# Kernel tuning notes

Measured on AMD Instinct MI355X. Metric: run time of the kernel, lower is better.

Reference implementation:

```python
import jax, jax.numpy as jnp
import numpy as np
from jax import lax

EMB, H1, H2 = 100, 128, 64  # embedding_dim, hidden_dim, hidden_dim//2
B, T = 1024, 512


def _uniform(key, shape, scale):
    return jax.random.uniform(key, shape, jnp.float32, -scale, scale)


def setup_inputs() -> dict:
    key = jax.random.key(0)
    ks = jax.random.split(key, 16)
    s1 = 1.0 / np.sqrt(H1)
    s2 = 1.0 / np.sqrt(H2)
    return {
        "X": jax.random.normal(ks[0], (B, T, EMB), jnp.float32),
        # PyTorch LSTM weights, gate order (i, f, g, o)
        "W1_ih": _uniform(ks[1], (4 * H1, EMB), s1),
        "W1_hh": _uniform(ks[2], (4 * H1, H1), s1),
        "b1_ih": _uniform(ks[3], (4 * H1,), s1),
        "b1_hh": _uniform(ks[4], (4 * H1,), s1),
        "W2_ih": _uniform(ks[5], (4 * H2, H1), s2),
        "W2_hh": _uniform(ks[6], (4 * H2, H2), s2),
        "b2_ih": _uniform(ks[7], (4 * H2,), s2),
        "b2_hh": _uniform(ks[8], (4 * H2,), s2),
        "fc1_w": _uniform(ks[9], (32, H2), 1.0 / np.sqrt(H2)),
        "fc1_b": _uniform(ks[10], (32,), 1.0 / np.sqrt(H2)),
        "fc2_w": _uniform(ks[11], (1, 32), 1.0 / np.sqrt(32)),
        "fc2_b": _uniform(ks[12], (1,), 1.0 / np.sqrt(32)),
    }


def _lstm(x, W_ih, W_hh, b_ih, b_hh):
    # x: [B, T, D]; returns (all hidden states [B, T, H], final h [B, H])
    Bb = x.shape[0]
    H = W_hh.shape[1]
    # Batch the input projection across all timesteps (one big GEMM).
    xw = jnp.einsum('btd,gd->tbg', x, W_ih) + (b_ih + b_hh)  # [T, B, 4H]

    def step(carry, xt):
        h, c = carry
        gates = xt + h @ W_hh.T  # [B, 4H]
        i, f, g, o = jnp.split(gates, 4, axis=-1)
        c = jax.nn.sigmoid(f) * c + jax.nn.sigmoid(i) * jnp.tanh(g)
        h = jax.nn.sigmoid(o) * jnp.tanh(c)
        return (h, c), h

    h0 = jnp.zeros((Bb, H), x.dtype)
    (h_n, _), hs = lax.scan(step, (h0, h0), xw)
    return jnp.swapaxes(hs, 0, 1), h_n


def reference(X, W1_ih, W1_hh, b1_ih, b1_hh,
              W2_ih, W2_hh, b2_ih, b2_hh,
              fc1_w, fc1_b, fc2_w, fc2_b):
    hs1, _ = _lstm(X, W1_ih, W1_hh, b1_ih, b1_hh)        # [B, T, 128]
    # dropout is identity at inference
    _, h_n = _lstm(hs1, W2_ih, W2_hh, b2_ih, b2_hh)      # [B, 64]
    x = jax.nn.relu(h_n @ fc1_w.T + fc1_b)               # [B, 32]
    x = x @ fc2_w.T + fc2_b                              # [B, 1]
    return jax.nn.sigmoid(x)[:, 0]                       # [B]
```

## Files before the change

### kernel.cpp

```cpp
#include <hip/hip_runtime.h>
#include <hip/hip_fp16.h>

typedef _Float16 half8 __attribute__((ext_vector_type(8)));
typedef _Float16 half4 __attribute__((ext_vector_type(4)));
typedef float floatx4 __attribute__((ext_vector_type(4)));

#define TT 512
#define EE 100
#define NBATCH 16
#define NBLK 64
#define WS_NEED ((size_t)NBLK * TT * 2048 * sizeof(_Float16))

typedef const __attribute__((address_space(1))) void gvoid_t;
typedef __attribute__((address_space(3))) void lvoid_t;

#define MFMA16 __builtin_amdgcn_mfma_f32_16x16x32_f16

__device__ __forceinline__ float sigm(float x) {
    return __builtin_amdgcn_rcpf(1.0f + __expf(-x));
}
__device__ __forceinline__ float tanh_(float x) {
    return __builtin_amdgcn_rcpf(1.0f + __expf(-2.0f * x)) * 2.0f - 1.0f;
}
__device__ __forceinline__ half4 cvt4(float4 v) {
    half4 h; h[0] = (_Float16)v.x; h[1] = (_Float16)v.y; h[2] = (_Float16)v.z; h[3] = (_Float16)v.w;
    return h;
}

extern "C" __global__ void __launch_bounds__(256)
xfrag_prep(const float* __restrict__ X, _Float16* __restrict__ xw)
{
    const int bt  = blockIdx.x;
    const int blk = bt >> 9;
    const int t   = bt & (TT - 1);
    const int tid = threadIdx.x;
    const int c   = tid >> 4, m = tid & 15;
    const int k0  = 8 * c;
    half8 v;
#pragma unroll
    for (int j = 0; j < 8; ++j) v[j] = (_Float16)0.0f;
    const float* p = X + ((size_t)(blk * 16 + m) * TT + t) * EE + k0;
    if (k0 + 8 <= EE) {
        float4 lo = *(const float4*)p;
        float4 hi = *(const float4*)(p + 4);
        v[0] = (_Float16)lo.x; v[1] = (_Float16)lo.y; v[2] = (_Float16)lo.z; v[3] = (_Float16)lo.w;
        v[4] = (_Float16)hi.x; v[5] = (_Float16)hi.y; v[6] = (_Float16)hi.z; v[7] = (_Float16)hi.w;
    } else if (k0 < EE) {
        float4 lo = *(const float4*)p;
        v[0] = (_Float16)lo.x; v[1] = (_Float16)lo.y; v[2] = (_Float16)lo.z; v[3] = (_Float16)lo.w;
        v[4] = (_Float16)1.0f;
    }
    *(half8*)&xw[(size_t)bt * 2048 + c * 128 + m * 8] = v;
}

template<int USE_WS>
__global__ void __launch_bounds__(512, 1)
lstm_mfma4(const float* __restrict__ X, const _Float16* __restrict__ xw,
           const float* __restrict__ W1ih, const float* __restrict__ W1hh,
           const float* __restrict__ b1i,  const float* __restrict__ b1h,
           const float* __restrict__ W2ih, const float* __restrict__ W2hh,
           const float* __restrict__ b2i,  const float* __restrict__ b2h,
           const float* __restrict__ fc1w, const float* __restrict__ fc1b,
           const float* __restrict__ fc2w, const float* __restrict__ fc2b,
           float* __restrict__ out)
{
    const int tid  = threadIdx.x;
    const int w    = tid >> 6;
    const int lane = tid & 63;
    const int q    = lane >> 4;
    const int m    = lane & 15;
    const int b0   = blockIdx.x * NBATCH;

    __shared__ __align__(16) _Float16 h1b[2][4][4][16][8];
    __shared__ __align__(16) _Float16 h2b[2][2][4][16][8];
    __shared__ __align__(16) _Float16 xb [2][4][4][16][8];
    __shared__ float fca[NBATCH][32];

    _Float16* const h1f = &h1b[0][0][0][0][0];
    _Float16* const h2f = &h2b[0][0][0][0][0];
    _Float16* const xbf = &xb [0][0][0][0][0];

    for (int i = tid; i < 2 * 2048; i += 512) h1f[i] = (_Float16)0.0f;
    for (int i = tid; i < 2 * 1024; i += 512) h2f[i] = (_Float16)0.0f;
    if (!USE_WS) {
        for (int i = tid; i < 2 * 2048; i += 512) {
            const int k = i & 2047;
            xbf[i] = (k >= 1536 && k < 1664 && (k & 7) == 4) ? (_Float16)1.0f
                                                             : (_Float16)0.0f;
        }
    }

    half8 w1ihf[4][4], w1hhf[4][4], w2ihf[2][4], w2hhf[2][2];
    floatx4 bias2v[2];
#pragma unroll
    for (int g = 0; g < 4; ++g) {
        const int r = g * 128 + 16 * w + m;
        const float bias = b1i[r] + b1h[r];
#pragma unroll
        for (int s = 0; s < 4; ++s) {
            half8 f;
#pragma unroll
            for (int j = 0; j < 8; ++j) {
                const int k = 32 * s + 8 * q + j;
                float v = 0.0f;
                if (k < EE) v = W1ih[r * EE + k];
                else if (k == EE) v = bias;
                f[j] = (_Float16)v;
            }
            w1ihf[g][s] = f;
        }
#pragma unroll
        for (int s = 0; s < 4; ++s) {
            half8 f;
#pragma unroll
            for (int j = 0; j < 8; ++j) f[j] = (_Float16)W1hh[r * 128 + 32 * s + 8 * q + j];
            w1hhf[g][s] = f;
        }
    }
#pragma unroll
    for (int tau = 0; tau < 2; ++tau) {
        const int rr = (m & 3) * 64 + 8 * w + 4 * tau + (m >> 2);
#pragma unroll
        for (int s = 0; s < 4; ++s) {
            half8 f;
#pragma unroll
            for (int j = 0; j < 8; ++j) f[j] = (_Float16)W2ih[rr * 128 + 32 * s + 8 * q + j];
            w2ihf[tau][s] = f;
        }
#pragma unroll
        for (int s = 0; s < 2; ++s) {
            half8 f;
#pragma unroll
            for (int j = 0; j < 8; ++j) f[j] = (_Float16)W2hh[rr * 64 + 32 * s + 8 * q + j];
            w2hhf[tau][s] = f;
        }
        const int uu = 8 * w + 4 * tau + q;
#pragma unroll
        for (int reg = 0; reg < 4; ++reg)
            bias2v[tau][reg] = b2i[reg * 64 + uu] + b2h[reg * 64 + uu];
    }

    const _Float16* xwb = xw + (size_t)blockIdx.x * TT * 2048;
    const int foff = q * 128 + m * 8;

    int gaddr = 0, laddr = 0;
    bool xval = false;
    float4 xr = {0.f, 0.f, 0.f, 0.f};
    if (!USE_WS) {
        xval = tid < 400;
        const int f = xval ? tid : 0;
        const int n = f / 25, pp = f - 25 * n, e0 = 4 * pp;
        gaddr = (b0 + n) * (TT * EE) + e0;
        const int s = e0 >> 5, qr = (e0 >> 3) & 3, j0 = e0 & 7;
        laddr = ((s * 4 + qr) * 16 + n) * 8 + j0;
    }

    __syncthreads();

    if (USE_WS) {
        if (w < 4) {
            __builtin_amdgcn_global_load_lds((gvoid_t*)(xwb + 0 * 2048 + w * 512 + lane * 8),
                                             (lvoid_t*)(xbf + 0 * 2048 + w * 512), 16, 0, 0);
            __builtin_amdgcn_global_load_lds((gvoid_t*)(xwb + 1 * 2048 + w * 512 + lane * 8),
                                             (lvoid_t*)(xbf + 1 * 2048 + w * 512), 16, 0, 0);
        }
    } else if (xval) {
        *(half4*)&xbf[0 * 2048 + laddr] = cvt4(*(const float4*)&X[gaddr + 0 * EE]);
        *(half4*)&xbf[1 * 2048 + laddr] = cvt4(*(const float4*)&X[gaddr + 1 * EE]);
        xr = *(const float4*)&X[gaddr + 2 * EE];
    }
    __syncthreads();

    floatx4 a1x[4];
#pragma unroll
    for (int g = 0; g < 4; ++g) a1x[g] = (floatx4){0.f, 0.f, 0.f, 0.f};
    {
        const _Float16* xc = xbf + 0 * 2048 + foff;
#pragma unroll
        for (int s = 0; s < 4; ++s) {
            half8 bx = *(const half8*)(xc + s * 512);
#pragma unroll
            for (int g = 0; g < 4; ++g) a1x[g] = MFMA16(w1ihf[g][s], bx, a1x[g], 0, 0, 0);
        }
    }

    floatx4 c1 = {0.f, 0.f, 0.f, 0.f};
    float c2[2] = {0.f, 0.f};
    const int vv = 2 * w + (q >> 1);
    const int jj = 4 * (q & 1);

#pragma unroll 1
    for (int t = 0; t < TT; ++t) {
        const int cur = t & 1, nxt = cur ^ 1;

        {
            const _Float16* hp = h1f + nxt * 2048 + foff;
#pragma unroll
            for (int s = 0; s < 4; ++s) {
                half8 bh = *(const half8*)(hp + s * 512);
#pragma unroll
                for (int g = 0; g < 4; ++g)
                    a1x[g] = MFMA16(w1hhf[g][s], bh, a1x[g], 0, 0, 0);
            }
        }
        {
            half4 hv;
#pragma unroll
            for (int r = 0; r < 4; ++r) {
                const float iv = sigm(a1x[0][r]);
                const float fv = sigm(a1x[1][r]);
                const float gv = tanh_(a1x[2][r]);
                const float ov = sigm(a1x[3][r]);
                const float c  = fv * c1[r] + iv * gv;
                c1[r] = c;
                hv[r] = (_Float16)(ov * tanh_(c));
            }
            *(half4*)&h1b[cur][vv >> 2][vv & 3][m][jj] = hv;
        }
        __syncthreads();

        if (USE_WS) {
            if (w < 4) {
                const int tn = (t + 2 < TT) ? (t + 2) : (TT - 1);
                __builtin_amdgcn_global_load_lds((gvoid_t*)(xwb + (size_t)tn * 2048 + w * 512 + lane * 8),
                                                 (lvoid_t*)(xbf + cur * 2048 + w * 512), 16, 0, 0);
            }
        } else if (xval) {
            *(half4*)&xbf[cur * 2048 + laddr] = cvt4(xr);
            const int tn = (t + 3 < TT) ? (t + 3) : (TT - 1);
            xr = *(const float4*)&X[gaddr + tn * EE];
        }

        floatx4 a2[2] = { bias2v[0], bias2v[1] };
        {
            const _Float16* hc = h1f + cur * 2048 + foff;
#pragma unroll
            for (int s = 0; s < 4; ++s) {
                half8 bh = *(const half8*)(hc + s * 512);
                a2[0] = MFMA16(w2ihf[0][s], bh, a2[0], 0, 0, 0);
                a2[1] = MFMA16(w2ihf[1][s], bh, a2[1], 0, 0, 0);
            }
            const _Float16* h2p = h2f + nxt * 1024 + foff;
#pragma unroll
            for (int s = 0; s < 2; ++s) {
                half8 b2v = *(const half8*)(h2p + s * 512);
                a2[0] = MFMA16(w2hhf[0][s], b2v, a2[0], 0, 0, 0);
                a2[1] = MFMA16(w2hhf[1][s], b2v, a2[1], 0, 0, 0);
            }
        }

        {
            const _Float16* xc = xbf + nxt * 2048 + foff;
#pragma unroll
            for (int g = 0; g < 4; ++g) a1x[g] = (floatx4){0.f, 0.f, 0.f, 0.f};
#pragma unroll
            for (int s = 0; s < 4; ++s) {
                half8 bx = *(const half8*)(xc + s * 512);
#pragma unroll
                for (int g = 0; g < 4; ++g)
                    a1x[g] = MFMA16(w1ihf[g][s], bx, a1x[g], 0, 0, 0);
            }
        }

#pragma unroll
        for (int tau = 0; tau < 2; ++tau) {
            const float iv = sigm(a2[tau][0]);
            const float fv = sigm(a2[tau][1]);
            const float gv = tanh_(a2[tau][2]);
            const float ov = sigm(a2[tau][3]);
            const float c  = fv * c2[tau] + iv * gv;
            c2[tau] = c;
            const int u = 8 * w + 4 * tau + q;
            h2f[cur * 1024 + (u >> 5) * 512 + ((u >> 3) & 3) * 128 + m * 8 + (u & 7)]
                = (_Float16)(ov * tanh_(c));
        }
    }
    __syncthreads();

    {
        const int nb = tid >> 5, o = tid & 31;
        float s = fc1b[o];
#pragma unroll
        for (int k = 0; k < 64; ++k)
            s += fc1w[o * 64 + k] * (float)h2b[1][k >> 5][(k >> 3) & 3][nb][k & 7];
        fca[nb][o] = fmaxf(s, 0.0f);
    }
    __syncthreads();
    if (tid < NBATCH) {
        float s = fc2b[0];
#pragma unroll
        for (int k = 0; k < 32; ++k) s += fc2w[k] * fca[tid][k];
        out[b0 + tid] = sigm(s);
    }
}

extern "C" void kernel_launch(void* const* d_in, const int* in_sizes, int n_in,
                              void* d_out, int out_size, void* d_ws, size_t ws_size,
                              hipStream_t stream) {
    const float* X    = (const float*)d_in[0];
    const float* W1ih = (const float*)d_in[1];
    const float* W1hh = (const float*)d_in[2];
    const float* b1i  = (const float*)d_in[3];
    const float* b1h  = (const float*)d_in[4];
    const float* W2ih = (const float*)d_in[5];
    const float* W2hh = (const float*)d_in[6];
    const float* b2i  = (const float*)d_in[7];
    const float* b2h  = (const float*)d_in[8];
    const float* fc1w = (const float*)d_in[9];
    const float* fc1b = (const float*)d_in[10];
    const float* fc2w = (const float*)d_in[11];
    const float* fc2b = (const float*)d_in[12];
    _Float16* xw = (_Float16*)d_ws;

    if (ws_size >= WS_NEED) {
        hipLaunchKernelGGL(xfrag_prep, dim3(NBLK * TT), dim3(256), 0, stream, X, xw);
        hipLaunchKernelGGL(lstm_mfma4<1>, dim3(NBLK), dim3(512), 0, stream,
                           X, xw, W1ih, W1hh, b1i, b1h, W2ih, W2hh, b2i, b2h,
                           fc1w, fc1b, fc2w, fc2b, (float*)d_out);
    } else {
        hipLaunchKernelGGL(lstm_mfma4<0>, dim3(NBLK), dim3(512), 0, stream,
                           X, xw, W1ih, W1hh, b1i, b1h, W2ih, W2hh, b2i, b2h,
                           fc1w, fc1b, fc2w, fc2b, (float*)d_out);
    }
}
```

Measured before the change: 1.128 ms.

## Interleave two independent batch groups per block to hide recurrence latency

Each block now runs two 16-sample batch groups (A and B) whose layer-1 and layer-2 steps are staggered by half a step, so independent MFMA and activation work from one group fills the dependency stalls of the other. This halves the grid to 32 blocks and keeps two barriers per step. The input-prep kernel is also rewritten to stage a 16-timestep tile in LDS so global reads of X are coalesced. The costs are more register pressure, only 32 of the GPU's compute units in use, and a longer serial instruction stream per block.

```diff
diff --git a/kernel.cpp b/kernel.cpp
--- a/kernel.cpp
+++ b/kernel.cpp
@@ -7,9 +7,8 @@
 
 #define TT 512
 #define EE 100
-#define NBATCH 16
-#define NBLK 64
-#define WS_NEED ((size_t)NBLK * TT * 2048 * sizeof(_Float16))
+#define NBLK 32
+#define WS_NEED ((size_t)64 * TT * 2048 * sizeof(_Float16))
 
 typedef const __attribute__((address_space(1))) void gvoid_t;
 typedef __attribute__((address_space(3))) void lvoid_t;
@@ -30,63 +29,148 @@
 extern "C" __global__ void __launch_bounds__(256)
 xfrag_prep(const float* __restrict__ X, _Float16* __restrict__ xw)
 {
-    const int bt  = blockIdx.x;
-    const int blk = bt >> 9;
-    const int t   = bt & (TT - 1);
+    const int g   = blockIdx.x >> 5;
+    const int t0  = (blockIdx.x & 31) << 4;
     const int tid = threadIdx.x;
-    const int c   = tid >> 4, m = tid & 15;
-    const int k0  = 8 * c;
-    half8 v;
-#pragma unroll
-    for (int j = 0; j < 8; ++j) v[j] = (_Float16)0.0f;
-    const float* p = X + ((size_t)(blk * 16 + m) * TT + t) * EE + k0;
-    if (k0 + 8 <= EE) {
-        float4 lo = *(const float4*)p;
-        float4 hi = *(const float4*)(p + 4);
-        v[0] = (_Float16)lo.x; v[1] = (_Float16)lo.y; v[2] = (_Float16)lo.z; v[3] = (_Float16)lo.w;
-        v[4] = (_Float16)hi.x; v[5] = (_Float16)hi.y; v[6] = (_Float16)hi.z; v[7] = (_Float16)hi.w;
-    } else if (k0 < EE) {
-        float4 lo = *(const float4*)p;
-        v[0] = (_Float16)lo.x; v[1] = (_Float16)lo.y; v[2] = (_Float16)lo.z; v[3] = (_Float16)lo.w;
-        v[4] = (_Float16)1.0f;
-    }
-    *(half8*)&xw[(size_t)bt * 2048 + c * 128 + m * 8] = v;
+
+    __shared__ __align__(16) _Float16 tile[16][16][120];
+
+    for (int mm = 0; mm < 16; ++mm) {
+        const float4* src = (const float4*)(X + ((size_t)(g * 16 + mm) * TT + t0) * EE);
+#pragma unroll
+        for (int r = 0; r < 2; ++r) {
+            const int idx = tid + r * 256;
+            if (idx < 400) {
+                float4 v = src[idx];
+                const int tt = idx / 25, kk = idx - 25 * tt;
+                *(half4*)&tile[tt][mm][4 * kk] = cvt4(v);
+            }
+        }
+    }
+    __syncthreads();
+
+    const int c = tid >> 4, mm = tid & 15;
+    for (int tt = 0; tt < 16; ++tt) {
+        half8 v;
+        if (c < 12) {
+            v = *(const half8*)&tile[tt][mm][8 * c];
+        } else if (c == 12) {
+            half4 lo = *(const half4*)&tile[tt][mm][96];
+            v[0] = lo[0]; v[1] = lo[1]; v[2] = lo[2]; v[3] = lo[3];
+            v[4] = (_Float16)1.0f;
+            v[5] = (_Float16)0.0f; v[6] = (_Float16)0.0f; v[7] = (_Float16)0.0f;
+        } else {
+#pragma unroll
+            for (int j = 0; j < 8; ++j) v[j] = (_Float16)0.0f;
+        }
+        *(half8*)&xw[((size_t)(g * TT) + t0 + tt) * 2048 + c * 128 + mm * 8] = v;
+    }
+}
+
+__device__ __forceinline__ void L1STEP(const _Float16* __restrict__ xslot,
+                                       const _Float16* __restrict__ hprev,
+                                       _Float16* __restrict__ hout,
+                                       floatx4& c1,
+                                       const half8 (&wih)[4][4], const half8 (&whh)[4][4],
+                                       int foff)
+{
+    floatx4 a[4];
+#pragma unroll
+    for (int gg = 0; gg < 4; ++gg) a[gg] = (floatx4){0.f, 0.f, 0.f, 0.f};
+#pragma unroll
+    for (int s = 0; s < 4; ++s) {
+        half8 bx = *(const half8*)(xslot + s * 512 + foff);
+#pragma unroll
+        for (int gg = 0; gg < 4; ++gg) a[gg] = MFMA16(wih[gg][s], bx, a[gg], 0, 0, 0);
+    }
+#pragma unroll
+    for (int s = 0; s < 4; ++s) {
+        half8 bh = *(const half8*)(hprev + s * 512 + foff);
+#pragma unroll
+        for (int gg = 0; gg < 4; ++gg) a[gg] = MFMA16(whh[gg][s], bh, a[gg], 0, 0, 0);
+    }
+    half4 hv;
+#pragma unroll
+    for (int r = 0; r < 4; ++r) {
+        const float iv = sigm(a[0][r]);
+        const float fv = sigm(a[1][r]);
+        const float gv = tanh_(a[2][r]);
+        const float ov = sigm(a[3][r]);
+        const float c  = fv * c1[r] + iv * gv;
+        c1[r] = c;
+        hv[r] = (_Float16)(ov * tanh_(c));
+    }
+    *(half4*)hout = hv;
+}
+
+__device__ __forceinline__ void L2STEP(const _Float16* __restrict__ h1cur,
+                                       const _Float16* __restrict__ h2prev,
+                                       _Float16* __restrict__ h2out_base,
+                                       const int (&uoff)[2],
+                                       float (&c2)[2],
+                                       const half8 (&wih)[2][4], const half8 (&whh)[2][2],
+                                       const floatx4 (&bias)[2],
+                                       int foff)
+{
+    floatx4 a2[2] = { bias[0], bias[1] };
+#pragma unroll
+    for (int s = 0; s < 4; ++s) {
+        half8 bh = *(const half8*)(h1cur + s * 512 + foff);
+        a2[0] = MFMA16(wih[0][s], bh, a2[0], 0, 0, 0);
+        a2[1] = MFMA16(wih[1][s], bh, a2[1], 0, 0, 0);
+    }
+#pragma unroll
+    for (int s = 0; s < 2; ++s) {
+        half8 bv = *(const half8*)(h2prev + s * 512 + foff);
+        a2[0] = MFMA16(whh[0][s], bv, a2[0], 0, 0, 0);
+        a2[1] = MFMA16(whh[1][s], bv, a2[1], 0, 0, 0);
+    }
+#pragma unroll
+    for (int tau = 0; tau < 2; ++tau) {
+        const float iv = sigm(a2[tau][0]);
+        const float fv = sigm(a2[tau][1]);
+        const float gv = tanh_(a2[tau][2]);
+        const float ov = sigm(a2[tau][3]);
+        const float c  = fv * c2[tau] + iv * gv;
+        c2[tau] = c;
+        h2out_base[uoff[tau]] = (_Float16)(ov * tanh_(c));
+    }
 }
 
 template<int USE_WS>
 __global__ void __launch_bounds__(512, 1)
-lstm_mfma4(const float* __restrict__ X, const _Float16* __restrict__ xw,
-           const float* __restrict__ W1ih, const float* __restrict__ W1hh,
-           const float* __restrict__ b1i,  const float* __restrict__ b1h,
-           const float* __restrict__ W2ih, const float* __restrict__ W2hh,
-           const float* __restrict__ b2i,  const float* __restrict__ b2h,
-           const float* __restrict__ fc1w, const float* __restrict__ fc1b,
-           const float* __restrict__ fc2w, const float* __restrict__ fc2b,
-           float* __restrict__ out)
+lstm_dual(const float* __restrict__ X, const _Float16* __restrict__ xw,
+          const float* __restrict__ W1ih, const float* __restrict__ W1hh,
+          const float* __restrict__ b1i,  const float* __restrict__ b1h,
+          const float* __restrict__ W2ih, const float* __restrict__ W2hh,
+          const float* __restrict__ b2i,  const float* __restrict__ b2h,
+          const float* __restrict__ fc1w, const float* __restrict__ fc1b,
+          const float* __restrict__ fc2w, const float* __restrict__ fc2b,
+          float* __restrict__ out)
 {
     const int tid  = threadIdx.x;
     const int w    = tid >> 6;
     const int lane = tid & 63;
     const int q    = lane >> 4;
     const int m    = lane & 15;
-    const int b0   = blockIdx.x * NBATCH;
-
-    __shared__ __align__(16) _Float16 h1b[2][4][4][16][8];
-    __shared__ __align__(16) _Float16 h2b[2][2][4][16][8];
-    __shared__ __align__(16) _Float16 xb [2][4][4][16][8];
-    __shared__ float fca[NBATCH][32];
-
-    _Float16* const h1f = &h1b[0][0][0][0][0];
-    _Float16* const h2f = &h2b[0][0][0][0][0];
-    _Float16* const xbf = &xb [0][0][0][0][0];
-
-    for (int i = tid; i < 2 * 2048; i += 512) h1f[i] = (_Float16)0.0f;
-    for (int i = tid; i < 2 * 1024; i += 512) h2f[i] = (_Float16)0.0f;
+    const int b0   = blockIdx.x * 32;
+
+    __shared__ __align__(16) _Float16 h1A[2 * 2048];
+    __shared__ __align__(16) _Float16 h1B[2 * 2048];
+    __shared__ __align__(16) _Float16 h2A[2 * 1024];
+    __shared__ __align__(16) _Float16 h2B[2 * 1024];
+    __shared__ __align__(16) _Float16 xbA[2 * 2048];
+    __shared__ __align__(16) _Float16 xbB[2 * 2048];
+    __shared__ float fca[32][32];
+
+    for (int i = tid; i < 2 * 2048; i += 512) { h1A[i] = (_Float16)0.0f; h1B[i] = (_Float16)0.0f; }
+    for (int i = tid; i < 2 * 1024; i += 512) { h2A[i] = (_Float16)0.0f; h2B[i] = (_Float16)0.0f; }
     if (!USE_WS) {
         for (int i = tid; i < 2 * 2048; i += 512) {
             const int k = i & 2047;
-            xbf[i] = (k >= 1536 && k < 1664 && (k & 7) == 4) ? (_Float16)1.0f
-                                                             : (_Float16)0.0f;
+            const _Float16 v = (k >= 1536 && k < 1664 && (k & 7) == 4) ? (_Float16)1.0f
+                                                                       : (_Float16)0.0f;
+            xbA[i] = v; xbB[i] = v;
         }
     }
 
@@ -140,17 +224,29 @@
             bias2v[tau][reg] = b2i[reg * 64 + uu] + b2h[reg * 64 + uu];
     }
 
-    const _Float16* xwb = xw + (size_t)blockIdx.x * TT * 2048;
-    const int foff = q * 128 + m * 8;
-
-    int gaddr = 0, laddr = 0;
+    const int foff  = q * 128 + m * 8;
+    const int vv    = 2 * w + (q >> 1);
+    const int jj    = 4 * (q & 1);
+    const int woff1 = (vv >> 2) * 512 + (vv & 3) * 128 + m * 8 + jj;
+    int uoff[2];
+#pragma unroll
+    for (int tau = 0; tau < 2; ++tau) {
+        const int u = 8 * w + 4 * tau + q;
+        uoff[tau] = (u >> 5) * 512 + ((u >> 3) & 3) * 128 + m * 8 + (u & 7);
+    }
+
+    const _Float16* xwbA = xw + (size_t)(2 * blockIdx.x)     * TT * 2048;
+    const _Float16* xwbB = xw + (size_t)(2 * blockIdx.x + 1) * TT * 2048;
+
+    int gaddrA = 0, gaddrB = 0, laddr = 0;
     bool xval = false;
-    float4 xr = {0.f, 0.f, 0.f, 0.f};
+    float4 xrA = {0.f, 0.f, 0.f, 0.f}, xrB = {0.f, 0.f, 0.f, 0.f};
     if (!USE_WS) {
         xval = tid < 400;
         const int f = xval ? tid : 0;
         const int n = f / 25, pp = f - 25 * n, e0 = 4 * pp;
-        gaddr = (b0 + n) * (TT * EE) + e0;
+        gaddrA = (b0 + n)      * (TT * EE) + e0;
+        gaddrB = (b0 + 16 + n) * (TT * EE) + e0;
         const int s = e0 >> 5, qr = (e0 >> 3) & 3, j0 = e0 & 7;
         laddr = ((s * 4 + qr) * 16 + n) * 8 + j0;
     }
@@ -159,134 +255,91 @@
 
     if (USE_WS) {
         if (w < 4) {
-            __builtin_amdgcn_global_load_lds((gvoid_t*)(xwb + 0 * 2048 + w * 512 + lane * 8),
-                                             (lvoid_t*)(xbf + 0 * 2048 + w * 512), 16, 0, 0);
-            __builtin_amdgcn_global_load_lds((gvoid_t*)(xwb + 1 * 2048 + w * 512 + lane * 8),
-                                             (lvoid_t*)(xbf + 1 * 2048 + w * 512), 16, 0, 0);
+            __builtin_amdgcn_global_load_lds((gvoid_t*)(xwbA + 0 * 2048 + w * 512 + lane * 8),
+                                             (lvoid_t*)(xbA + 0 * 2048 + w * 512), 16, 0, 0);
+            __builtin_amdgcn_global_load_lds((gvoid_t*)(xwbA + 1 * 2048 + w * 512 + lane * 8),
+                                             (lvoid_t*)(xbA + 1 * 2048 + w * 512), 16, 0, 0);
+        } else {
+            const int wb = w - 4;
+            __builtin_amdgcn_global_load_lds((gvoid_t*)(xwbB + 0 * 2048 + wb * 512 + lane * 8),
+                                             (lvoid_t*)(xbB + 0 * 2048 + wb * 512), 16, 0, 0);
+            __builtin_amdgcn_global_load_lds((gvoid_t*)(xwbB + 1 * 2048 + wb * 512 + lane * 8),
+                                             (lvoid_t*)(xbB + 1 * 2048 + wb * 512), 16, 0, 0);
         }
     } else if (xval) {
-        *(half4*)&xbf[0 * 2048 + laddr] = cvt4(*(const float4*)&X[gaddr + 0 * EE]);
-        *(half4*)&xbf[1 * 2048 + laddr] = cvt4(*(const float4*)&X[gaddr + 1 * EE]);
-        xr = *(const float4*)&X[gaddr + 2 * EE];
-    }
-    __syncthreads();
-
-    floatx4 a1x[4];
-#pragma unroll
-    for (int g = 0; g < 4; ++g) a1x[g] = (floatx4){0.f, 0.f, 0.f, 0.f};
-    {
-        const _Float16* xc = xbf + 0 * 2048 + foff;
-#pragma unroll
-        for (int s = 0; s < 4; ++s) {
-            half8 bx = *(const half8*)(xc + s * 512);
-#pragma unroll
-            for (int g = 0; g < 4; ++g) a1x[g] = MFMA16(w1ihf[g][s], bx, a1x[g], 0, 0, 0);
-        }
-    }
-
-    floatx4 c1 = {0.f, 0.f, 0.f, 0.f};
-    float c2[2] = {0.f, 0.f};
-    const int vv = 2 * w + (q >> 1);
-    const int jj = 4 * (q & 1);
+        *(half4*)&xbA[0 * 2048 + laddr] = cvt4(*(const float4*)&X[gaddrA + 0 * EE]);
+        *(half4*)&xbA[1 * 2048 + laddr] = cvt4(*(const float4*)&X[gaddrA + 1 * EE]);
+        *(half4*)&xbB[0 * 2048 + laddr] = cvt4(*(const float4*)&X[gaddrB + 0 * EE]);
+        *(half4*)&xbB[1 * 2048 + laddr] = cvt4(*(const float4*)&X[gaddrB + 1 * EE]);
+        xrA = *(const float4*)&X[gaddrA + 2 * EE];
+        xrB = *(const float4*)&X[gaddrB + 2 * EE];
+    }
+    __syncthreads();
+
+    floatx4 c1A = {0.f, 0.f, 0.f, 0.f};
+    floatx4 c1B = {0.f, 0.f, 0.f, 0.f};
+    float c2A[2] = {0.f, 0.f};
+    float c2B[2] = {0.f, 0.f};
 
 #pragma unroll 1
-    for (int t = 0; t < TT; ++t) {
-        const int cur = t & 1, nxt = cur ^ 1;
-
-        {
-            const _Float16* hp = h1f + nxt * 2048 + foff;
-#pragma unroll
-            for (int s = 0; s < 4; ++s) {
-                half8 bh = *(const half8*)(hp + s * 512);
-#pragma unroll
-                for (int g = 0; g < 4; ++g)
-                    a1x[g] = MFMA16(w1hhf[g][s], bh, a1x[g], 0, 0, 0);
+    for (int p = 0; p < TT; ++p) {
+        const int cur = p & 1, nxt = cur ^ 1;
+
+        L1STEP(xbA + cur * 2048, h1A + nxt * 2048,
+               h1A + cur * 2048 + woff1, c1A, w1ihf, w1hhf, foff);
+        if (p >= 1) {
+            L2STEP(h1B + nxt * 2048, h2B + cur * 1024,
+                   h2B + nxt * 1024, uoff, c2B, w2ihf, w2hhf, bias2v, foff);
+            if (USE_WS) {
+                if (w >= 4) {
+                    const int tn = (p + 1 < TT) ? (p + 1) : (TT - 1);
+                    const int wb = w - 4;
+                    __builtin_amdgcn_global_load_lds((gvoid_t*)(xwbB + (size_t)tn * 2048 + wb * 512 + lane * 8),
+                                                     (lvoid_t*)(xbB + nxt * 2048 + wb * 512), 16, 0, 0);
+                }
+            } else if (xval) {
+                *(half4*)&xbB[nxt * 2048 + laddr] = cvt4(xrB);
+                const int tn = (p + 2 < TT) ? (p + 2) : (TT - 1);
+                xrB = *(const float4*)&X[gaddrB + tn * EE];
             }
         }
-        {
-            half4 hv;
-#pragma unroll
-            for (int r = 0; r < 4; ++r) {
-                const float iv = sigm(a1x[0][r]);
-                const float fv = sigm(a1x[1][r]);
-                const float gv = tanh_(a1x[2][r]);
-                const float ov = sigm(a1x[3][r]);
-                const float c  = fv * c1[r] + iv * gv;
-                c1[r] = c;
-                hv[r] = (_Float16)(ov * tanh_(c));
-            }
-            *(half4*)&h1b[cur][vv >> 2][vv & 3][m][jj] = hv;
-        }
         __syncthreads();
 
+        L2STEP(h1A + cur * 2048, h2A + nxt * 1024,
+               h2A + cur * 1024, uoff, c2A, w2ihf, w2hhf, bias2v, foff);
+        L1STEP(xbB + cur * 2048, h1B + nxt * 2048,
+               h1B + cur * 2048 + woff1, c1B, w1ihf, w1hhf, foff);
         if (USE_WS) {
             if (w < 4) {
-                const int tn = (t + 2 < TT) ? (t + 2) : (TT - 1);
-                __builtin_amdgcn_global_load_lds((gvoid_t*)(xwb + (size_t)tn * 2048 + w * 512 + lane * 8),
-                                                 (lvoid_t*)(xbf + cur * 2048 + w * 512), 16, 0, 0);
+                const int tn = (p + 2 < TT) ? (p + 2) : (TT - 1);
+                __builtin_amdgcn_global_load_lds((gvoid_t*)(xwbA + (size_t)tn * 2048 + w * 512 + lane * 8),
+                                                 (lvoid_t*)(xbA + cur * 2048 + w * 512), 16, 0, 0);
             }
         } else if (xval) {
-            *(half4*)&xbf[cur * 2048 + laddr] = cvt4(xr);
-            const int tn = (t + 3 < TT) ? (t + 3) : (TT - 1);
-            xr = *(const float4*)&X[gaddr + tn * EE];
-        }
-
-        floatx4 a2[2] = { bias2v[0], bias2v[1] };
-        {
-            const _Float16* hc = h1f + cur * 2048 + foff;
-#pragma unroll
-            for (int s = 0; s < 4; ++s) {
-                half8 bh = *(const half8*)(hc + s * 512);
-                a2[0] = MFMA16(w2ihf[0][s], bh, a2[0], 0, 0, 0);
-                a2[1] = MFMA16(w2ihf[1][s], bh, a2[1], 0, 0, 0);
-            }
-            const _Float16* h2p = h2f + nxt * 1024 + foff;
-#pragma unroll
-            for (int s = 0; s < 2; ++s) {
-                half8 b2v = *(const half8*)(h2p + s * 512);
-                a2[0] = MFMA16(w2hhf[0][s], b2v, a2[0], 0, 0, 0);
-                a2[1] = MFMA16(w2hhf[1][s], b2v, a2[1], 0, 0, 0);
-            }
-        }
-
-        {
-            const _Float16* xc = xbf + nxt * 2048 + foff;
-#pragma unroll
-            for (int g = 0; g < 4; ++g) a1x[g] = (floatx4){0.f, 0.f, 0.f, 0.f};
-#pragma unroll
-            for (int s = 0; s < 4; ++s) {
-                half8 bx = *(const half8*)(xc + s * 512);
-#pragma unroll
-                for (int g = 0; g < 4; ++g)
-                    a1x[g] = MFMA16(w1ihf[g][s], bx, a1x[g], 0, 0, 0);
-            }
-        }
-
-#pragma unroll
-        for (int tau = 0; tau < 2; ++tau) {
-            const float iv = sigm(a2[tau][0]);
-            const float fv = sigm(a2[tau][1]);
-            const float gv = tanh_(a2[tau][2]);
-            const float ov = sigm(a2[tau][3]);
-            const float c  = fv * c2[tau] + iv * gv;
-            c2[tau] = c;
-            const int u = 8 * w + 4 * tau + q;
-            h2f[cur * 1024 + (u >> 5) * 512 + ((u >> 3) & 3) * 128 + m * 8 + (u & 7)]
-                = (_Float16)(ov * tanh_(c));
-        }
-    }
-    __syncthreads();
-
-    {
-        const int nb = tid >> 5, o = tid & 31;
+            *(half4*)&xbA[cur * 2048 + laddr] = cvt4(xrA);
+            const int tn = (p + 3 < TT) ? (p + 3) : (TT - 1);
+            xrA = *(const float4*)&X[gaddrA + tn * EE];
+        }
+        __syncthreads();
+    }
+
+    L2STEP(h1B + 1 * 2048, h2B + 0 * 1024,
+           h2B + 1 * 1024, uoff, c2B, w2ihf, w2hhf, bias2v, foff);
+    __syncthreads();
+
+#pragma unroll
+    for (int rep = 0; rep < 2; ++rep) {
+        const int idx = tid + rep * 512;
+        const int nb = idx >> 5, o = idx & 31;
+        const _Float16* h2p = (nb < 16 ? h2A : h2B) + 1024 + (nb & 15) * 8;
         float s = fc1b[o];
 #pragma unroll
         for (int k = 0; k < 64; ++k)
-            s += fc1w[o * 64 + k] * (float)h2b[1][k >> 5][(k >> 3) & 3][nb][k & 7];
+            s += fc1w[o * 64 + k] * (float)h2p[(k >> 5) * 512 + ((k >> 3) & 3) * 128 + (k & 7)];
         fca[nb][o] = fmaxf(s, 0.0f);
     }
     __syncthreads();
-    if (tid < NBATCH) {
+    if (tid < 32) {
         float s = fc2b[0];
 #pragma unroll
         for (int k = 0; k < 32; ++k) s += fc2w[k] * fca[tid][k];
@@ -313,12 +366,12 @@
     _Float16* xw = (_Float16*)d_ws;
 
     if (ws_size >= WS_NEED) {
-        hipLaunchKernelGGL(xfrag_prep, dim3(NBLK * TT), dim3(256), 0, stream, X, xw);
-        hipLaunchKernelGGL(lstm_mfma4<1>, dim3(NBLK), dim3(512), 0, stream,
+        hipLaunchKernelGGL(xfrag_prep, dim3(2048), dim3(256), 0, stream, X, xw);
+        hipLaunchKernelGGL(lstm_dual<1>, dim3(NBLK), dim3(512), 0, stream,
                            X, xw, W1ih, W1hh, b1i, b1h, W2ih, W2hh, b2i, b2h,
                            fc1w, fc1b, fc2w, fc2b, (float*)d_out);
     } else {
-        hipLaunchKernelGGL(lstm_mfma4<0>, dim3(NBLK), dim3(512), 0, stream,
+        hipLaunchKernelGGL(lstm_dual<0>, dim3(NBLK), dim3(512), 0, stream,
                            X, xw, W1ih, W1hh, b1i, b1h, W2ih, W2hh, b2i, b2h,
                            fc1w, fc1b, fc2w, fc2b, (float*)d_out);
     }
```

Measured after the change: 2.085 ms. 84.9% more time.

## Tile X prep through LDS and keep LSTM MFMA operands in registers

Applied to the files above, without the earlier changes.

The prep kernel now has each block load 16 timesteps for 16 batch rows into a shared-memory tile with contiguous float4 reads, then writes the fragment layout. Previously each block handled a single timestep with strided loads. In the recurrent kernel, the h1, h2 and x fragments for the next step are loaded from LDS into registers right after the barrier. The layer-1 input projection and recurrent MFMAs then run together at the top of the step instead of the input projection being precomputed at the end of the previous step. This shortens the dependency chain between LDS reads and MFMAs on the critical path, but it raises register pressure and moves the input-projection MFMAs back onto the serial recurrence.

```diff
diff --git a/kernel.cpp b/kernel.cpp
--- a/kernel.cpp
+++ b/kernel.cpp
@@ -30,39 +30,54 @@
 extern "C" __global__ void __launch_bounds__(256)
 xfrag_prep(const float* __restrict__ X, _Float16* __restrict__ xw)
 {
-    const int bt  = blockIdx.x;
-    const int blk = bt >> 9;
-    const int t   = bt & (TT - 1);
+    const int g   = blockIdx.x >> 5;
+    const int t0  = (blockIdx.x & 31) << 4;
     const int tid = threadIdx.x;
-    const int c   = tid >> 4, m = tid & 15;
-    const int k0  = 8 * c;
-    half8 v;
-#pragma unroll
-    for (int j = 0; j < 8; ++j) v[j] = (_Float16)0.0f;
-    const float* p = X + ((size_t)(blk * 16 + m) * TT + t) * EE + k0;
-    if (k0 + 8 <= EE) {
-        float4 lo = *(const float4*)p;
-        float4 hi = *(const float4*)(p + 4);
-        v[0] = (_Float16)lo.x; v[1] = (_Float16)lo.y; v[2] = (_Float16)lo.z; v[3] = (_Float16)lo.w;
-        v[4] = (_Float16)hi.x; v[5] = (_Float16)hi.y; v[6] = (_Float16)hi.z; v[7] = (_Float16)hi.w;
-    } else if (k0 < EE) {
-        float4 lo = *(const float4*)p;
-        v[0] = (_Float16)lo.x; v[1] = (_Float16)lo.y; v[2] = (_Float16)lo.z; v[3] = (_Float16)lo.w;
-        v[4] = (_Float16)1.0f;
-    }
-    *(half8*)&xw[(size_t)bt * 2048 + c * 128 + m * 8] = v;
+
+    __shared__ __align__(16) _Float16 tile[16][16][120];
+
+    for (int mm = 0; mm < 16; ++mm) {
+        const float4* src = (const float4*)(X + ((size_t)(g * 16 + mm) * TT + t0) * EE);
+#pragma unroll
+        for (int r = 0; r < 2; ++r) {
+            const int idx = tid + r * 256;
+            if (idx < 400) {
+                float4 v = src[idx];
+                const int tt = idx / 25, kk = idx - 25 * tt;
+                *(half4*)&tile[tt][mm][4 * kk] = cvt4(v);
+            }
+        }
+    }
+    __syncthreads();
+
+    const int c = tid >> 4, mm = tid & 15;
+    for (int tt = 0; tt < 16; ++tt) {
+        half8 v;
+        if (c < 12) {
+            v = *(const half8*)&tile[tt][mm][8 * c];
+        } else if (c == 12) {
+            half4 lo = *(const half4*)&tile[tt][mm][96];
+            v[0] = lo[0]; v[1] = lo[1]; v[2] = lo[2]; v[3] = lo[3];
+            v[4] = (_Float16)1.0f;
+            v[5] = (_Float16)0.0f; v[6] = (_Float16)0.0f; v[7] = (_Float16)0.0f;
+        } else {
+#pragma unroll
+            for (int j = 0; j < 8; ++j) v[j] = (_Float16)0.0f;
+        }
+        *(half8*)&xw[((size_t)(g * TT) + t0 + tt) * 2048 + c * 128 + mm * 8] = v;
+    }
 }
 
 template<int USE_WS>
 __global__ void __launch_bounds__(512, 1)
-lstm_mfma4(const float* __restrict__ X, const _Float16* __restrict__ xw,
-           const float* __restrict__ W1ih, const float* __restrict__ W1hh,
-           const float* __restrict__ b1i,  const float* __restrict__ b1h,
-           const float* __restrict__ W2ih, const float* __restrict__ W2hh,
-           const float* __restrict__ b2i,  const float* __restrict__ b2h,
-           const float* __restrict__ fc1w, const float* __restrict__ fc1b,
-           const float* __restrict__ fc2w, const float* __restrict__ fc2b,
-           float* __restrict__ out)
+lstm_regc(const float* __restrict__ X, const _Float16* __restrict__ xw,
+          const float* __restrict__ W1ih, const float* __restrict__ W1hh,
+          const float* __restrict__ b1i,  const float* __restrict__ b1h,
+          const float* __restrict__ W2ih, const float* __restrict__ W2hh,
+          const float* __restrict__ b2i,  const float* __restrict__ b2h,
+          const float* __restrict__ fc1w, const float* __restrict__ fc1b,
+          const float* __restrict__ fc2w, const float* __restrict__ fc2b,
+          float* __restrict__ out)
 {
     const int tid  = threadIdx.x;
     const int w    = tid >> 6;
@@ -71,22 +86,17 @@
     const int m    = lane & 15;
     const int b0   = blockIdx.x * NBATCH;
 
-    __shared__ __align__(16) _Float16 h1b[2][4][4][16][8];
-    __shared__ __align__(16) _Float16 h2b[2][2][4][16][8];
-    __shared__ __align__(16) _Float16 xb [2][4][4][16][8];
+    __shared__ __align__(16) _Float16 h1b[2 * 2048];
+    __shared__ __align__(16) _Float16 h2b[2 * 1024];
+    __shared__ __align__(16) _Float16 xb [2 * 2048];
     __shared__ float fca[NBATCH][32];
 
-    _Float16* const h1f = &h1b[0][0][0][0][0];
-    _Float16* const h2f = &h2b[0][0][0][0][0];
-    _Float16* const xbf = &xb [0][0][0][0][0];
-
-    for (int i = tid; i < 2 * 2048; i += 512) h1f[i] = (_Float16)0.0f;
-    for (int i = tid; i < 2 * 1024; i += 512) h2f[i] = (_Float16)0.0f;
+    for (int i = tid; i < 2 * 1024; i += 512) h2b[i] = (_Float16)0.0f;
     if (!USE_WS) {
         for (int i = tid; i < 2 * 2048; i += 512) {
             const int k = i & 2047;
-            xbf[i] = (k >= 1536 && k < 1664 && (k & 7) == 4) ? (_Float16)1.0f
-                                                             : (_Float16)0.0f;
+            xb[i] = (k >= 1536 && k < 1664 && (k & 7) == 4) ? (_Float16)1.0f
+                                                            : (_Float16)0.0f;
         }
     }
 
@@ -140,8 +150,18 @@
             bias2v[tau][reg] = b2i[reg * 64 + uu] + b2h[reg * 64 + uu];
     }
 
+    const int foff  = q * 128 + m * 8;
+    const int vv    = 2 * w + (q >> 1);
+    const int jj    = 4 * (q & 1);
+    const int woff1 = (vv >> 2) * 512 + (vv & 3) * 128 + m * 8 + jj;
+    int uoff[2];
+#pragma unroll
+    for (int tau = 0; tau < 2; ++tau) {
+        const int u = 8 * w + 4 * tau + q;
+        uoff[tau] = (u >> 5) * 512 + ((u >> 3) & 3) * 128 + m * 8 + (u & 7);
+    }
+
     const _Float16* xwb = xw + (size_t)blockIdx.x * TT * 2048;
-    const int foff = q * 128 + m * 8;
 
     int gaddr = 0, laddr = 0;
     bool xval = false;
@@ -160,62 +180,58 @@
     if (USE_WS) {
         if (w < 4) {
             __builtin_amdgcn_global_load_lds((gvoid_t*)(xwb + 0 * 2048 + w * 512 + lane * 8),
-                                             (lvoid_t*)(xbf + 0 * 2048 + w * 512), 16, 0, 0);
+                                             (lvoid_t*)(xb + 0 * 2048 + w * 512), 16, 0, 0);
             __builtin_amdgcn_global_load_lds((gvoid_t*)(xwb + 1 * 2048 + w * 512 + lane * 8),
-                                             (lvoid_t*)(xbf + 1 * 2048 + w * 512), 16, 0, 0);
+                                             (lvoid_t*)(xb + 1 * 2048 + w * 512), 16, 0, 0);
         }
     } else if (xval) {
-        *(half4*)&xbf[0 * 2048 + laddr] = cvt4(*(const float4*)&X[gaddr + 0 * EE]);
-        *(half4*)&xbf[1 * 2048 + laddr] = cvt4(*(const float4*)&X[gaddr + 1 * EE]);
+        *(half4*)&xb[0 * 2048 + laddr] = cvt4(*(const float4*)&X[gaddr + 0 * EE]);
+        *(half4*)&xb[1 * 2048 + laddr] = cvt4(*(const float4*)&X[gaddr + 1 * EE]);
         xr = *(const float4*)&X[gaddr + 2 * EE];
     }
     __syncthreads();
 
-    floatx4 a1x[4];
-#pragma unroll
-    for (int g = 0; g < 4; ++g) a1x[g] = (floatx4){0.f, 0.f, 0.f, 0.f};
-    {
-        const _Float16* xc = xbf + 0 * 2048 + foff;
-#pragma unroll
-        for (int s = 0; s < 4; ++s) {
-            half8 bx = *(const half8*)(xc + s * 512);
-#pragma unroll
-            for (int g = 0; g < 4; ++g) a1x[g] = MFMA16(w1ihf[g][s], bx, a1x[g], 0, 0, 0);
-        }
+    half8 bx[4], bh[4];
+#pragma unroll
+    for (int s = 0; s < 4; ++s) {
+        bx[s] = *(const half8*)(xb + 0 * 2048 + s * 512 + foff);
+#pragma unroll
+        for (int j = 0; j < 8; ++j) bh[s][j] = (_Float16)0.0f;
     }
 
     floatx4 c1 = {0.f, 0.f, 0.f, 0.f};
     float c2[2] = {0.f, 0.f};
-    const int vv = 2 * w + (q >> 1);
-    const int jj = 4 * (q & 1);
 
 #pragma unroll 1
     for (int t = 0; t < TT; ++t) {
         const int cur = t & 1, nxt = cur ^ 1;
 
         {
-            const _Float16* hp = h1f + nxt * 2048 + foff;
+            floatx4 a[4];
+#pragma unroll
+            for (int g = 0; g < 4; ++g) a[g] = (floatx4){0.f, 0.f, 0.f, 0.f};
 #pragma unroll
             for (int s = 0; s < 4; ++s) {
-                half8 bh = *(const half8*)(hp + s * 512);
-#pragma unroll
-                for (int g = 0; g < 4; ++g)
-                    a1x[g] = MFMA16(w1hhf[g][s], bh, a1x[g], 0, 0, 0);
-            }
-        }
-        {
+#pragma unroll
+                for (int g = 0; g < 4; ++g) a[g] = MFMA16(w1ihf[g][s], bx[s], a[g], 0, 0, 0);
+            }
+#pragma unroll
+            for (int s = 0; s < 4; ++s) {
+#pragma unroll
+                for (int g = 0; g < 4; ++g) a[g] = MFMA16(w1hhf[g][s], bh[s], a[g], 0, 0, 0);
+            }
             half4 hv;
 #pragma unroll
             for (int r = 0; r < 4; ++r) {
-                const float iv = sigm(a1x[0][r]);
-                const float fv = sigm(a1x[1][r]);
-                const float gv = tanh_(a1x[2][r]);
-                const float ov = sigm(a1x[3][r]);
+                const float iv = sigm(a[0][r]);
+                const float fv = sigm(a[1][r]);
+                const float gv = tanh_(a[2][r]);
+                const float ov = sigm(a[3][r]);
                 const float c  = fv * c1[r] + iv * gv;
                 c1[r] = c;
                 hv[r] = (_Float16)(ov * tanh_(c));
             }
-            *(half4*)&h1b[cur][vv >> 2][vv & 3][m][jj] = hv;
+            *(half4*)&h1b[cur * 2048 + woff1] = hv;
         }
         __syncthreads();
 
@@ -223,43 +239,32 @@
             if (w < 4) {
                 const int tn = (t + 2 < TT) ? (t + 2) : (TT - 1);
                 __builtin_amdgcn_global_load_lds((gvoid_t*)(xwb + (size_t)tn * 2048 + w * 512 + lane * 8),
-                                                 (lvoid_t*)(xbf + cur * 2048 + w * 512), 16, 0, 0);
+                                                 (lvoid_t*)(xb + cur * 2048 + w * 512), 16, 0, 0);
             }
         } else if (xval) {
-            *(half4*)&xbf[cur * 2048 + laddr] = cvt4(xr);
+            *(half4*)&xb[cur * 2048 + laddr] = cvt4(xr);
             const int tn = (t + 3 < TT) ? (t + 3) : (TT - 1);
             xr = *(const float4*)&X[gaddr + tn * EE];
         }
 
+        half8 h2f[2];
+#pragma unroll
+        for (int s = 0; s < 4; ++s) bh[s] = *(const half8*)(h1b + cur * 2048 + s * 512 + foff);
+#pragma unroll
+        for (int s = 0; s < 2; ++s) h2f[s] = *(const half8*)(h2b + nxt * 1024 + s * 512 + foff);
+#pragma unroll
+        for (int s = 0; s < 4; ++s) bx[s] = *(const half8*)(xb + nxt * 2048 + s * 512 + foff);
+
         floatx4 a2[2] = { bias2v[0], bias2v[1] };
-        {
-            const _Float16* hc = h1f + cur * 2048 + foff;
-#pragma unroll
-            for (int s = 0; s < 4; ++s) {
-                half8 bh = *(const half8*)(hc + s * 512);
-                a2[0] = MFMA16(w2ihf[0][s], bh, a2[0], 0, 0, 0);
-                a2[1] = MFMA16(w2ihf[1][s], bh, a2[1], 0, 0, 0);
-            }
-            const _Float16* h2p = h2f + nxt * 1024 + foff;
-#pragma unroll
-            for (int s = 0; s < 2; ++s) {
-                half8 b2v = *(const half8*)(h2p + s * 512);
-                a2[0] = MFMA16(w2hhf[0][s], b2v, a2[0], 0, 0, 0);
-                a2[1] = MFMA16(w2hhf[1][s], b2v, a2[1], 0, 0, 0);
-            }
-        }
-
-        {
-            const _Float16* xc = xbf + nxt * 2048 + foff;
-#pragma unroll
-            for (int g = 0; g < 4; ++g) a1x[g] = (floatx4){0.f, 0.f, 0.f, 0.f};
-#pragma unroll
-            for (int s = 0; s < 4; ++s) {
-                half8 bx = *(const half8*)(xc + s * 512);
-#pragma unroll
-                for (int g = 0; g < 4; ++g)
-                    a1x[g] = MFMA16(w1ihf[g][s], bx, a1x[g], 0, 0, 0);
-            }
+#pragma unroll
+        for (int s = 0; s < 4; ++s) {
+            a2[0] = MFMA16(w2ihf[0][s], bh[s], a2[0], 0, 0, 0);
+            a2[1] = MFMA16(w2ihf[1][s], bh[s], a2[1], 0, 0, 0);
+        }
+#pragma unroll
+        for (int s = 0; s < 2; ++s) {
+            a2[0] = MFMA16(w2hhf[0][s], h2f[s], a2[0], 0, 0, 0);
+            a2[1] = MFMA16(w2hhf[1][s], h2f[s], a2[1], 0, 0, 0);
         }
 
 #pragma unroll
@@ -270,19 +275,18 @@
             const float ov = sigm(a2[tau][3]);
             const float c  = fv * c2[tau] + iv * gv;
             c2[tau] = c;
-            const int u = 8 * w + 4 * tau + q;
-            h2f[cur * 1024 + (u >> 5) * 512 + ((u >> 3) & 3) * 128 + m * 8 + (u & 7)]
-                = (_Float16)(ov * tanh_(c));
+            h2b[cur * 1024 + uoff[tau]] = (_Float16)(ov * tanh_(c));
         }
     }
     __syncthreads();
 
     {
         const int nb = tid >> 5, o = tid & 31;
+        const _Float16* h2p = h2b + 1024 + nb * 8;
         float s = fc1b[o];
 #pragma unroll
         for (int k = 0; k < 64; ++k)
-            s += fc1w[o * 64 + k] * (float)h2b[1][k >> 5][(k >> 3) & 3][nb][k & 7];
+            s += fc1w[o * 64 + k] * (float)h2p[(k >> 5) * 512 + ((k >> 3) & 3) * 128 + (k & 7)];
         fca[nb][o] = fmaxf(s, 0.0f);
     }
     __syncthreads();
@@ -313,12 +317,12 @@
     _Float16* xw = (_Float16*)d_ws;
 
     if (ws_size >= WS_NEED) {
-        hipLaunchKernelGGL(xfrag_prep, dim3(NBLK * TT), dim3(256), 0, stream, X, xw);
-        hipLaunchKernelGGL(lstm_mfma4<1>, dim3(NBLK), dim3(512), 0, stream,
+        hipLaunchKernelGGL(xfrag_prep, dim3(2048), dim3(256), 0, stream, X, xw);
+        hipLaunchKernelGGL(lstm_regc<1>, dim3(NBLK), dim3(512), 0, stream,
                            X, xw, W1ih, W1hh, b1i, b1h, W2ih, W2hh, b2i, b2h,
                            fc1w, fc1b, fc2w, fc2b, (float*)d_out);
     } else {
-        hipLaunchKernelGGL(lstm_mfma4<0>, dim3(NBLK), dim3(512), 0, stream,
+        hipLaunchKernelGGL(lstm_regc<0>, dim3(NBLK), dim3(512), 0, stream,
                            X, xw, W1ih, W1hh, b1i, b1h, W2ih, W2hh, b2i, b2h,
                            fc1w, fc1b, fc2w, fc2b, (float*)d_out);
     }
```

Result: no change. 1.129 ms (+0.1%).
